# Optimization experiments

Hardware: AMD Instinct MI355X
Metric: run time of the kernel (lower is better)

Reference implementation:

```python
import jax, jax.numpy as jnp
import numpy as np

B, M, D, H = 2, 2048, 1024, 16


def _rope(x):
    # Equivalent to x.transpose(0,1) @ R[:m] with R the block-diagonal 2x2
    # rotation matrices from get_rotary_matrix (note the (i-1) in theta,
    # faithful to the source).
    b, m, d = x.shape
    i = jnp.arange(d // 2, dtype=jnp.float32)
    theta = 10000.0 ** (-2.0 * (i - 1.0) / d)           # [d/2]
    ang = jnp.arange(m, dtype=jnp.float32)[:, None] * theta[None, :]  # [m, d/2]
    c, s = jnp.cos(ang), jnp.sin(ang)
    xe, xo = x[..., 0::2], x[..., 1::2]                 # [b, m, d/2]
    ye = xe * c + xo * s                                # out[2i]   = q[2i]*cos + q[2i+1]*sin
    yo = -xe * s + xo * c                               # out[2i+1] = -q[2i]*sin + q[2i+1]*cos
    return jnp.stack([ye, yo], axis=-1).reshape(b, m, d)


def setup_inputs() -> dict:
    key = jax.random.key(0)
    ks = jax.random.split(key, 8)
    w = lambda k, shape: (jax.random.normal(k, shape, jnp.float32) * 0.02)
    return {
        "x": jax.random.normal(ks[0], (B, M, D), jnp.float32),
        "wq": w(ks[1], (D, D)),
        "wk": w(ks[2], (D, D)),
        "wv": w(ks[3], (D, D)),
        "in_proj_w": w(ks[4], (3 * D, D)),
        "in_proj_b": w(ks[5], (3 * D,)),
        "out_w": w(ks[6], (D, D)),
        "out_b": w(ks[7], (D,)),
    }


def reference(x, wq, wk, wv, in_proj_w, in_proj_b, out_w, out_b):
    b, m, d = x.shape
    h = H
    hd = d // h
    # bias-free QKV projections, each followed by the dense RoPE rotation
    q = _rope(x @ wq.T)
    k = _rope(x @ wk.T)
    v = _rope(x @ wv.T)
    # nn.MultiheadAttention: packed in_proj, scaled dot-product, causal mask, out_proj
    wqi, wki, wvi = jnp.split(in_proj_w, 3, axis=0)
    bqi, bki, bvi = jnp.split(in_proj_b, 3, axis=0)
    qh = (q @ wqi.T + bqi).reshape(b, m, h, hd)
    kh = (k @ wki.T + bki).reshape(b, m, h, hd)
    vh = (v @ wvi.T + bvi).reshape(b, m, h, hd)
    scores = jnp.einsum("bqhd,bkhd->bhqk", qh, kh) / jnp.sqrt(jnp.float32(hd))
    causal = jnp.tril(jnp.ones((m, m), dtype=bool))
    scores = jnp.where(causal, scores, jnp.float32(-jnp.inf))
    attn = jax.nn.softmax(scores, axis=-1)              # dropout p=0.0
    o = jnp.einsum("bhqk,bkhd->bqhd", attn, vh).reshape(b, m, d)
    return o @ out_w.T + out_b
```

## Files before the change

### kernel.cpp

```cpp
#include <hip/hip_runtime.h>
#include <hip/hip_bf16.h>
#include <math.h>

typedef __bf16 bf16;
typedef __bf16 bf16x4 __attribute__((ext_vector_type(4)));
typedef __bf16 bf16x8 __attribute__((ext_vector_type(8)));
typedef float  f32x4  __attribute__((ext_vector_type(4)));

#define MM 2048
#define DD 1024
#define HD 64

__device__ __forceinline__ void gload16(const void* g, void* l) {
  __builtin_amdgcn_global_load_lds((const __attribute__((address_space(1))) void*)g,
                                   (__attribute__((address_space(3))) void*)l, 16, 0, 0);
}

__global__ __launch_bounds__(256) void k_cvt_all(
    const float* __restrict__ x,   const float* __restrict__ wq,
    const float* __restrict__ wk,  const float* __restrict__ wv,
    const float* __restrict__ ipw, const float* __restrict__ ow,
    bf16* __restrict__ xb,  bf16* __restrict__ wqb, bf16* __restrict__ wkb,
    bf16* __restrict__ wvb, bf16* __restrict__ ipwb, bf16* __restrict__ owb)
{
  int bid = blockIdx.x;
  const float* s; bf16* d; int base;
  if (bid < 4096)       { s = x;   d = xb;   base = bid; }
  else if (bid < 5120)  { s = wq;  d = wqb;  base = bid - 4096; }
  else if (bid < 6144)  { s = wk;  d = wkb;  base = bid - 5120; }
  else if (bid < 7168)  { s = wv;  d = wvb;  base = bid - 6144; }
  else if (bid < 10240) { s = ipw; d = ipwb; base = bid - 7168; }
  else                  { s = ow;  d = owb;  base = bid - 10240; }
  int i = base*256 + threadIdx.x;
  float4 v = ((const float4*)s)[i];
  bf16x4 o;
  o[0]=(bf16)v.x; o[1]=(bf16)v.y; o[2]=(bf16)v.z; o[3]=(bf16)v.w;
  ((bf16x4*)d)[i] = o;
}

__device__ __forceinline__ void gemm_core(const bf16* __restrict__ A,
                                          const bf16* __restrict__ Bw,
                                          const int row0, const int col0,
                                          bf16* __restrict__ sA, bf16* __restrict__ sB,
                                          f32x4 (&acc)[4][4])
{
  const int t = threadIdx.x;
  #pragma unroll
  for (int m=0;m<4;m++)
    #pragma unroll
    for (int n=0;n<4;n++)
      acc[m][n] = (f32x4){0.f,0.f,0.f,0.f};

  const int srow = t >> 3;
  const int lch  = ((t & 7) - (srow & 7)) & 7;
  const bf16* gA = A  + (size_t)(row0 + srow)*DD + lch*8;
  const bf16* gB = Bw + (size_t)(col0 + srow)*DD + lch*8;
  char* lA = (char*)sA + t*16;
  char* lB = (char*)sB + t*16;

  const int lane = t & 63, wid = t >> 6;
  const int wr = wid >> 1, wc = wid & 1;
  const int fr = lane & 15, fg = lane >> 4;
  const int fr7 = fr & 7;

  #pragma unroll
  for (int jj=0;jj<4;jj++) gload16(gA + (size_t)jj*32*DD, lA + jj*4096);
  #pragma unroll
  for (int jj=0;jj<4;jj++) gload16(gB + (size_t)jj*32*DD, lB + jj*4096);

  for (int kt = 0; kt < 16; ++kt) {
    const int buf = kt & 1;
    __builtin_amdgcn_s_barrier();
    if (kt < 15) {
      const int nb = buf ^ 1;
      const int ko = (kt + 1) * 64;
      #pragma unroll
      for (int jj=0;jj<4;jj++) gload16(gA + (size_t)jj*32*DD + ko, lA + nb*16384 + jj*4096);
      #pragma unroll
      for (int jj=0;jj<4;jj++) gload16(gB + (size_t)jj*32*DD + ko, lB + nb*16384 + jj*4096);
      asm volatile("s_waitcnt vmcnt(8)" ::: "memory");
    } else {
      asm volatile("s_waitcnt vmcnt(0)" ::: "memory");
    }
    __builtin_amdgcn_s_barrier();
    const char* bA = (const char*)sA + buf*16384;
    const char* bB = (const char*)sB + buf*16384;
    bf16x8 aF[2][4], bF[2][4];
    #pragma unroll
    for (int kb=0;kb<2;kb++) {
      #pragma unroll
      for (int m=0;m<4;m++)
        aF[kb][m] = *(const bf16x8*)(bA + (wr*64 + m*16 + fr)*128 + ((kb*4 + fg + fr7)&7)*16);
      #pragma unroll
      for (int n=0;n<4;n++)
        bF[kb][n] = *(const bf16x8*)(bB + (wc*64 + n*16 + fr)*128 + ((kb*4 + fg + fr7)&7)*16);
    }
    __builtin_amdgcn_s_setprio(1);
    #pragma unroll
    for (int kb=0;kb<2;kb++)
      #pragma unroll
      for (int m=0;m<4;m++)
        #pragma unroll
        for (int n=0;n<4;n++)
          acc[m][n] = __builtin_amdgcn_mfma_f32_16x16x32_bf16(aF[kb][m], bF[kb][n], acc[m][n], 0, 0, 0);
    __builtin_amdgcn_s_setprio(0);
  }
}

__global__ __launch_bounds__(256, 2) void k_gemm_rope(
    const bf16* __restrict__ X, const bf16* __restrict__ Wq,
    const bf16* __restrict__ Wk, const bf16* __restrict__ Wv,
    bf16* __restrict__ QKV)
{
  __shared__ bf16 sA[2*128*64];
  __shared__ bf16 sB[2*128*64];
  const int row0 = blockIdx.x * 128;
  const int col0 = blockIdx.y * 128;
  const int z = blockIdx.z;
  const bf16* Bw = (z==0) ? Wq : ((z==1) ? Wk : Wv);
  f32x4 acc[4][4];
  gemm_core(X, Bw, row0, col0, sA, sB, acc);

  bf16* outp = QKV + (size_t)z * (4096u*1024u);
  const int lane = threadIdx.x & 63, wid = threadIdx.x >> 6;
  const int wr = wid >> 1, wc = wid & 1;
  const int fr = lane & 15, fg = lane >> 4;
  #pragma unroll
  for (int n=0;n<4;n++) {
    const int gc = col0 + wc*64 + n*16 + fr;
    const int i2 = gc >> 1;
    const float theta = __expf(((float)i2 - 1.0f) * (-2.0f * 9.210340371976184f / 1024.0f));
    #pragma unroll
    for (int m=0;m<4;m++) {
      #pragma unroll
      for (int r=0;r<4;r++) {
        const int gr = row0 + wr*64 + m*16 + fg*4 + r;
        const float v  = acc[m][n][r];
        const float pv = __shfl_xor(v, 1);
        const int pos = gr & (MM-1);
        float sv, cv;
        __sincosf((float)pos * theta, &sv, &cv);
        const float res = (gc & 1) ? (v*cv - pv*sv) : (v*cv + pv*sv);
        outp[(size_t)gr * DD + gc] = (bf16)res;
      }
    }
  }
}

__global__ __launch_bounds__(256, 2) void k_gemm_proj(
    const bf16* __restrict__ QKV, const bf16* __restrict__ IPW,
    const float* __restrict__ IPB,
    bf16* __restrict__ QH, bf16* __restrict__ KH, bf16* __restrict__ VT)
{
  __shared__ bf16 sA[2*128*64];
  __shared__ bf16 sB[2*128*64];
  const int row0 = blockIdx.x * 128;
  const int col0 = blockIdx.y * 128;
  const int z = blockIdx.z;
  const bf16* A  = QKV + (size_t)z * (4096u*1024u);
  const bf16* Bw = IPW + (size_t)z * (1024u*1024u);
  const float* bias = IPB + z * DD;
  f32x4 acc[4][4];
  gemm_core(A, Bw, row0, col0, sA, sB, acc);

  const int lane = threadIdx.x & 63, wid = threadIdx.x >> 6;
  const int wr = wid >> 1, wc = wid & 1;
  const int fr = lane & 15, fg = lane >> 4;
  if (z < 2) {
    bf16* outp = (z==0) ? QH : KH;
    const float vscale = (z==0) ? 0.18033688011112042f : 1.0f;
    #pragma unroll
    for (int n=0;n<4;n++) {
      const int gc = col0 + wc*64 + n*16 + fr;
      const float bs = bias[gc];
      #pragma unroll
      for (int m=0;m<4;m++) {
        #pragma unroll
        for (int r=0;r<4;r++) {
          const int gr = row0 + wr*64 + m*16 + fg*4 + r;
          outp[(size_t)gr * DD + gc] = (bf16)((acc[m][n][r] + bs) * vscale);
        }
      }
    }
  } else {
    #pragma unroll
    for (int n=0;n<4;n++) {
      const int gc = col0 + wc*64 + n*16 + fr;
      const float bs = bias[gc];
      #pragma unroll
      for (int m=0;m<4;m++) {
        const int gr0 = row0 + wr*64 + m*16 + fg*4;
        const int b  = gr0 >> 11;
        const int m0 = gr0 & (MM-1);
        bf16x4 pk;
        #pragma unroll
        for (int r=0;r<4;r++) pk[r] = (bf16)(acc[m][n][r] + bs);
        *(bf16x4*)(VT + ((size_t)b*DD + gc)*MM + m0) = pk;
      }
    }
  }
}

__global__ __launch_bounds__(256) void k_attn(
    const bf16* __restrict__ QH, const bf16* __restrict__ KH,
    const bf16* __restrict__ VT, bf16* __restrict__ O)
{
  __shared__ bf16 sK[2*64*64];
  __shared__ bf16 sV[2*64*64];
  __shared__ bf16 sP[4*16*64];
  const int idx = blockIdx.x;
  const int xcd = idx & 7;
  const int rr  = idx >> 3;
  const int combo = xcd*4 + (rr & 3);
  const int b = combo >> 4, h = combo & 15;
  const int pair = rr >> 2;
  const int t = threadIdx.x, lane = t & 63, wid = t >> 6;
  const int fr = lane & 15, fg = lane >> 4;
  const int swzP = (fr & 7) << 4;

  const int srow = t >> 3;
  const int cc   = (t & 7) ^ (srow & 7);
  const bf16* gK0 = KH + ((size_t)b*MM + srow)*DD + h*HD + cc*8;
  const bf16* gK1 = gK0 + (size_t)32*DD;
  const bf16* gV0 = VT + ((size_t)b*DD + h*HD + srow)*MM + cc*8;
  const bf16* gV1 = gV0 + (size_t)32*MM;
  char* lK = (char*)sK + t*16;
  char* lV = (char*)sV + t*16;
  char* sPw = (char*)(sP + wid*16*64);

  #pragma unroll 1
  for (int half = 0; half < 2; ++half) {
    const int qt = half ? pair : (31 - pair);
    const int q0 = qt * 64;
    const int qg = q0 + wid*16 + fr;

    const bf16* qp = QH + ((size_t)b*MM + qg)*DD + h*HD + fg*8;
    bf16x8 aQ0 = *(const bf16x8*)qp;
    bf16x8 aQ1 = *(const bf16x8*)(qp + 32);

    if (half) __builtin_amdgcn_s_barrier();

    gload16(gK0, lK);  gload16(gK1, lK + 4096);
    gload16(gV0, lV);  gload16(gV1, lV + 4096);

    f32x4 o_acc[4];
    #pragma unroll
    for (int n=0;n<4;n++) o_acc[n] = (f32x4){0.f,0.f,0.f,0.f};
    float mrow = -INFINITY, lrow = 0.f;

    for (int kt = 0; kt <= qt; ++kt) {
      const int buf = kt & 1;
      asm volatile("s_waitcnt vmcnt(0)" ::: "memory");
      __builtin_amdgcn_s_barrier();
      if (kt < qt) {
        const int nb = buf ^ 1;
        gload16(gK0 + (size_t)(kt+1)*64*DD, lK + nb*8192);
        gload16(gK1 + (size_t)(kt+1)*64*DD, lK + nb*8192 + 4096);
        gload16(gV0 + (kt+1)*64,            lV + nb*8192);
        gload16(gV1 + (kt+1)*64,            lV + nb*8192 + 4096);
      }
      const char* bKb = (const char*)sK + buf*8192;
      const char* bVb = (const char*)sV + buf*8192;

      f32x4 sacc[4];
      #pragma unroll
      for (int n=0;n<4;n++) sacc[n] = (f32x4){0.f,0.f,0.f,0.f};
      __builtin_amdgcn_s_setprio(1);
      #pragma unroll
      for (int kb=0;kb<2;kb++) {
        const bf16x8 q = kb ? aQ1 : aQ0;
        #pragma unroll
        for (int n=0;n<4;n++) {
          const int rowA = n*16 + fr;
          bf16x8 aK = *(const bf16x8*)(bKb + rowA*128 + ((kb*64 + fg*16) ^ ((rowA&7)<<4)));
          sacc[n] = __builtin_amdgcn_mfma_f32_16x16x32_bf16(aK, q, sacc[n], 0, 0, 0);
        }
      }
      __builtin_amdgcn_s_setprio(0);

      const bool diag = (kt == qt);
      float pv[16];
      #pragma unroll
      for (int n=0;n<4;n++)
        #pragma unroll
        for (int r=0;r<4;r++) {
          float xx = sacc[n][r];
          if (diag) {
            const int kvg = kt*64 + n*16 + fg*4 + r;
            if (kvg > qg) xx = -INFINITY;
          }
          pv[n*4+r] = xx;
        }
      float m8[8];
      #pragma unroll
      for (int i=0;i<8;i++) m8[i] = fmaxf(pv[i], pv[i+8]);
      #pragma unroll
      for (int i=0;i<4;i++) m8[i] = fmaxf(m8[i], m8[i+4]);
      float rmax = fmaxf(fmaxf(m8[0],m8[1]), fmaxf(m8[2],m8[3]));
      rmax = fmaxf(rmax, __shfl_xor(rmax, 16));
      rmax = fmaxf(rmax, __shfl_xor(rmax, 32));
      if (!__all(rmax - mrow <= 11.5f)) {
        const float mnew = fmaxf(mrow, rmax);
        const float scale = exp2f(mrow - mnew);
        mrow = mnew;
        lrow *= scale;
        float sc[4];
        #pragma unroll
        for (int r=0;r<4;r++) sc[r] = __shfl(scale, fg*4 + r);
        #pragma unroll
        for (int n=0;n<4;n++)
          #pragma unroll
          for (int r=0;r<4;r++) o_acc[n][r] *= sc[r];
      }
      float ps[16];
      #pragma unroll
      for (int i=0;i<16;i++) ps[i] = exp2f(pv[i] - mrow);
      #pragma unroll
      for (int n=0;n<4;n++) {
        bf16x4 pk;
        #pragma unroll
        for (int r=0;r<4;r++) pk[r] = (bf16)ps[n*4+r];
        *(bf16x4*)(sPw + fr*128 + ((n*32 + fg*8) ^ swzP)) = pk;
      }
      float s8[8];
      #pragma unroll
      for (int i=0;i<8;i++) s8[i] = ps[i] + ps[i+8];
      #pragma unroll
      for (int i=0;i<4;i++) s8[i] += s8[i+4];
      float rsum = (s8[0]+s8[1]) + (s8[2]+s8[3]);
      rsum += __shfl_xor(rsum, 16);
      rsum += __shfl_xor(rsum, 32);
      lrow += rsum;
      asm volatile("s_waitcnt lgkmcnt(0)" ::: "memory");

      bf16x8 aP0 = *(const bf16x8*)(sPw + fr*128 + ((fg*16) ^ swzP));
      bf16x8 aP1 = *(const bf16x8*)(sPw + fr*128 + ((64 + fg*16) ^ swzP));
      __builtin_amdgcn_s_setprio(1);
      #pragma unroll
      for (int n=0;n<4;n++) {
        const int rowV = n*16 + fr;
        bf16x8 bV0 = *(const bf16x8*)(bVb + rowV*128 + ((fg*16) ^ ((rowV&7)<<4)));
        bf16x8 bV1 = *(const bf16x8*)(bVb + rowV*128 + ((64 + fg*16) ^ ((rowV&7)<<4)));
        o_acc[n] = __builtin_amdgcn_mfma_f32_16x16x32_bf16(aP0, bV0, o_acc[n], 0, 0, 0);
        o_acc[n] = __builtin_amdgcn_mfma_f32_16x16x32_bf16(aP1, bV1, o_acc[n], 0, 0, 0);
      }
      __builtin_amdgcn_s_setprio(0);
    }

    const float linv = 1.0f / lrow;
    float inv4[4];
    #pragma unroll
    for (int r=0;r<4;r++) inv4[r] = __shfl(linv, fg*4 + r);
    #pragma unroll
    for (int r=0;r<4;r++) {
      const int qq = q0 + wid*16 + fg*4 + r;
      #pragma unroll
      for (int n=0;n<4;n++) {
        O[((size_t)b*MM + qq)*DD + h*HD + n*16 + fr] = (bf16)(o_acc[n][r] * inv4[r]);
      }
    }
  }
}

__global__ __launch_bounds__(256, 2) void k_gemm_out(
    const bf16* __restrict__ A, const bf16* __restrict__ OW,
    const float* __restrict__ OBIAS, float* __restrict__ outp)
{
  __shared__ bf16 sA[2*128*64];
  __shared__ bf16 sB[2*128*64];
  const int row0 = blockIdx.x * 128;
  const int col0 = blockIdx.y * 128;
  f32x4 acc[4][4];
  gemm_core(A, OW, row0, col0, sA, sB, acc);
  const int lane = threadIdx.x & 63, wid = threadIdx.x >> 6;
  const int wr = wid >> 1, wc = wid & 1;
  const int fr = lane & 15, fg = lane >> 4;
  #pragma unroll
  for (int n=0;n<4;n++) {
    const int gc = col0 + wc*64 + n*16 + fr;
    const float bs = OBIAS[gc];
    #pragma unroll
    for (int m=0;m<4;m++) {
      #pragma unroll
      for (int r=0;r<4;r++) {
        const int gr = row0 + wr*64 + m*16 + fg*4 + r;
        outp[(size_t)gr * DD + gc] = acc[m][n][r] + bs;
      }
    }
  }
}

extern "C" void kernel_launch(void* const* d_in, const int* in_sizes, int n_in,
                              void* d_out, int out_size, void* d_ws, size_t ws_size,
                              hipStream_t stream)
{
  (void)in_sizes; (void)n_in; (void)out_size; (void)ws_size;
  const float* x   = (const float*)d_in[0];
  const float* wq  = (const float*)d_in[1];
  const float* wk  = (const float*)d_in[2];
  const float* wv  = (const float*)d_in[3];
  const float* ipw = (const float*)d_in[4];
  const float* ipb = (const float*)d_in[5];
  const float* ow  = (const float*)d_in[6];
  const float* ob  = (const float*)d_in[7];
  float* outp = (float*)d_out;

  char* ws = (char*)d_ws;
  const size_t MB = 1u << 20;
  bf16* xb   = (bf16*)(ws + 0*MB);
  bf16* wqb  = (bf16*)(ws + 8*MB);
  bf16* wkb  = (bf16*)(ws + 10*MB);
  bf16* wvb  = (bf16*)(ws + 12*MB);
  bf16* ipwb = (bf16*)(ws + 14*MB);
  bf16* owb  = (bf16*)(ws + 20*MB);
  bf16* QKV  = (bf16*)(ws + 22*MB);
  bf16* QH   = (bf16*)(ws + 46*MB);
  bf16* KH   = (bf16*)(ws + 54*MB);
  bf16* VT   = (bf16*)(ws + 62*MB);
  bf16* Ob   = (bf16*)(ws + 70*MB);

  k_cvt_all<<<11264, 256, 0, stream>>>(x, wq, wk, wv, ipw, ow,
                                       xb, wqb, wkb, wvb, ipwb, owb);
  k_gemm_rope<<<dim3(32,8,3), 256, 0, stream>>>(xb, wqb, wkb, wvb, QKV);
  k_gemm_proj<<<dim3(32,8,3), 256, 0, stream>>>(QKV, ipwb, ipb, QH, KH, VT);
  k_attn<<<512, 256, 0, stream>>>(QH, KH, VT, Ob);
  k_gemm_out<<<dim3(32,8,1), 256, 0, stream>>>(Ob, owb, ob, outp);
}
```

Baseline: 157.8 us.

## Use 8-wave GEMM blocks and one query tile per attention block

The shared GEMM core now runs with 512 threads (8 waves) per 128x128 tile. Each wave computes a 32x64 sub-tile instead of 64x64, and each thread issues half as many global-to-LDS loads per stage. The attention kernel no longer pairs a long and a short causal query tile in one block; it launches 1024 blocks, each handling a single query tile in descending tile order. The aim is more waves in flight and finer-grained scheduling, at the cost of less register-level reuse per wave in the GEMMs and the loss of the explicit causal load balancing from pairing.

```diff
diff --git a/kernel.cpp b/kernel.cpp
--- a/kernel.cpp
+++ b/kernel.cpp
@@ -38,15 +38,15 @@
   ((bf16x4*)d)[i] = o;
 }
 
-__device__ __forceinline__ void gemm_core(const bf16* __restrict__ A,
-                                          const bf16* __restrict__ Bw,
-                                          const int row0, const int col0,
-                                          bf16* __restrict__ sA, bf16* __restrict__ sB,
-                                          f32x4 (&acc)[4][4])
+__device__ __forceinline__ void gemm_core8(const bf16* __restrict__ A,
+                                           const bf16* __restrict__ Bw,
+                                           const int row0, const int col0,
+                                           bf16* __restrict__ sA, bf16* __restrict__ sB,
+                                           f32x4 (&acc)[2][4])
 {
   const int t = threadIdx.x;
   #pragma unroll
-  for (int m=0;m<4;m++)
+  for (int m=0;m<2;m++)
     #pragma unroll
     for (int n=0;n<4;n++)
       acc[m][n] = (f32x4){0.f,0.f,0.f,0.f};
@@ -63,10 +63,10 @@
   const int fr = lane & 15, fg = lane >> 4;
   const int fr7 = fr & 7;
 
-  #pragma unroll
-  for (int jj=0;jj<4;jj++) gload16(gA + (size_t)jj*32*DD, lA + jj*4096);
-  #pragma unroll
-  for (int jj=0;jj<4;jj++) gload16(gB + (size_t)jj*32*DD, lB + jj*4096);
+  gload16(gA,                 lA);
+  gload16(gA + (size_t)64*DD, lA + 8192);
+  gload16(gB,                 lB);
+  gload16(gB + (size_t)64*DD, lB + 8192);
 
   for (int kt = 0; kt < 16; ++kt) {
     const int buf = kt & 1;
@@ -74,23 +74,23 @@
     if (kt < 15) {
       const int nb = buf ^ 1;
       const int ko = (kt + 1) * 64;
-      #pragma unroll
-      for (int jj=0;jj<4;jj++) gload16(gA + (size_t)jj*32*DD + ko, lA + nb*16384 + jj*4096);
-      #pragma unroll
-      for (int jj=0;jj<4;jj++) gload16(gB + (size_t)jj*32*DD + ko, lB + nb*16384 + jj*4096);
-      asm volatile("s_waitcnt vmcnt(8)" ::: "memory");
+      gload16(gA + ko,                 lA + nb*16384);
+      gload16(gA + (size_t)64*DD + ko, lA + nb*16384 + 8192);
+      gload16(gB + ko,                 lB + nb*16384);
+      gload16(gB + (size_t)64*DD + ko, lB + nb*16384 + 8192);
+      asm volatile("s_waitcnt vmcnt(4)" ::: "memory");
     } else {
       asm volatile("s_waitcnt vmcnt(0)" ::: "memory");
     }
     __builtin_amdgcn_s_barrier();
     const char* bA = (const char*)sA + buf*16384;
     const char* bB = (const char*)sB + buf*16384;
-    bf16x8 aF[2][4], bF[2][4];
+    bf16x8 aF[2][2], bF[2][4];
     #pragma unroll
     for (int kb=0;kb<2;kb++) {
       #pragma unroll
-      for (int m=0;m<4;m++)
-        aF[kb][m] = *(const bf16x8*)(bA + (wr*64 + m*16 + fr)*128 + ((kb*4 + fg + fr7)&7)*16);
+      for (int m=0;m<2;m++)
+        aF[kb][m] = *(const bf16x8*)(bA + (wr*32 + m*16 + fr)*128 + ((kb*4 + fg + fr7)&7)*16);
       #pragma unroll
       for (int n=0;n<4;n++)
         bF[kb][n] = *(const bf16x8*)(bB + (wc*64 + n*16 + fr)*128 + ((kb*4 + fg + fr7)&7)*16);
@@ -99,7 +99,7 @@
     #pragma unroll
     for (int kb=0;kb<2;kb++)
       #pragma unroll
-      for (int m=0;m<4;m++)
+      for (int m=0;m<2;m++)
         #pragma unroll
         for (int n=0;n<4;n++)
           acc[m][n] = __builtin_amdgcn_mfma_f32_16x16x32_bf16(aF[kb][m], bF[kb][n], acc[m][n], 0, 0, 0);
@@ -107,7 +107,7 @@
   }
 }
 
-__global__ __launch_bounds__(256, 2) void k_gemm_rope(
+__global__ __launch_bounds__(512, 2) void k_gemm_rope(
     const bf16* __restrict__ X, const bf16* __restrict__ Wq,
     const bf16* __restrict__ Wk, const bf16* __restrict__ Wv,
     bf16* __restrict__ QKV)
@@ -118,8 +118,8 @@
   const int col0 = blockIdx.y * 128;
   const int z = blockIdx.z;
   const bf16* Bw = (z==0) ? Wq : ((z==1) ? Wk : Wv);
-  f32x4 acc[4][4];
-  gemm_core(X, Bw, row0, col0, sA, sB, acc);
+  f32x4 acc[2][4];
+  gemm_core8(X, Bw, row0, col0, sA, sB, acc);
 
   bf16* outp = QKV + (size_t)z * (4096u*1024u);
   const int lane = threadIdx.x & 63, wid = threadIdx.x >> 6;
@@ -131,10 +131,10 @@
     const int i2 = gc >> 1;
     const float theta = __expf(((float)i2 - 1.0f) * (-2.0f * 9.210340371976184f / 1024.0f));
     #pragma unroll
-    for (int m=0;m<4;m++) {
+    for (int m=0;m<2;m++) {
       #pragma unroll
       for (int r=0;r<4;r++) {
-        const int gr = row0 + wr*64 + m*16 + fg*4 + r;
+        const int gr = row0 + wr*32 + m*16 + fg*4 + r;
         const float v  = acc[m][n][r];
         const float pv = __shfl_xor(v, 1);
         const int pos = gr & (MM-1);
@@ -147,7 +147,7 @@
   }
 }
 
-__global__ __launch_bounds__(256, 2) void k_gemm_proj(
+__global__ __launch_bounds__(512, 2) void k_gemm_proj(
     const bf16* __restrict__ QKV, const bf16* __restrict__ IPW,
     const float* __restrict__ IPB,
     bf16* __restrict__ QH, bf16* __restrict__ KH, bf16* __restrict__ VT)
@@ -160,8 +160,8 @@
   const bf16* A  = QKV + (size_t)z * (4096u*1024u);
   const bf16* Bw = IPW + (size_t)z * (1024u*1024u);
   const float* bias = IPB + z * DD;
-  f32x4 acc[4][4];
-  gemm_core(A, Bw, row0, col0, sA, sB, acc);
+  f32x4 acc[2][4];
+  gemm_core8(A, Bw, row0, col0, sA, sB, acc);
 
   const int lane = threadIdx.x & 63, wid = threadIdx.x >> 6;
   const int wr = wid >> 1, wc = wid & 1;
@@ -174,10 +174,10 @@
       const int gc = col0 + wc*64 + n*16 + fr;
       const float bs = bias[gc];
       #pragma unroll
-      for (int m=0;m<4;m++) {
+      for (int m=0;m<2;m++) {
         #pragma unroll
         for (int r=0;r<4;r++) {
-          const int gr = row0 + wr*64 + m*16 + fg*4 + r;
+          const int gr = row0 + wr*32 + m*16 + fg*4 + r;
           outp[(size_t)gr * DD + gc] = (bf16)((acc[m][n][r] + bs) * vscale);
         }
       }
@@ -188,8 +188,8 @@
       const int gc = col0 + wc*64 + n*16 + fr;
       const float bs = bias[gc];
       #pragma unroll
-      for (int m=0;m<4;m++) {
-        const int gr0 = row0 + wr*64 + m*16 + fg*4;
+      for (int m=0;m<2;m++) {
+        const int gr0 = row0 + wr*32 + m*16 + fg*4;
         const int b  = gr0 >> 11;
         const int m0 = gr0 & (MM-1);
         bf16x4 pk;
@@ -213,10 +213,12 @@
   const int rr  = idx >> 3;
   const int combo = xcd*4 + (rr & 3);
   const int b = combo >> 4, h = combo & 15;
-  const int pair = rr >> 2;
+  const int qt = 31 - (rr >> 2);
   const int t = threadIdx.x, lane = t & 63, wid = t >> 6;
   const int fr = lane & 15, fg = lane >> 4;
   const int swzP = (fr & 7) << 4;
+  const int q0 = qt * 64;
+  const int qg = q0 + wid*16 + fr;
 
   const int srow = t >> 3;
   const int cc   = (t & 7) ^ (srow & 7);
@@ -228,141 +230,132 @@
   char* lV = (char*)sV + t*16;
   char* sPw = (char*)(sP + wid*16*64);
 
-  #pragma unroll 1
-  for (int half = 0; half < 2; ++half) {
-    const int qt = half ? pair : (31 - pair);
-    const int q0 = qt * 64;
-    const int qg = q0 + wid*16 + fr;
-
-    const bf16* qp = QH + ((size_t)b*MM + qg)*DD + h*HD + fg*8;
-    bf16x8 aQ0 = *(const bf16x8*)qp;
-    bf16x8 aQ1 = *(const bf16x8*)(qp + 32);
-
-    if (half) __builtin_amdgcn_s_barrier();
-
-    gload16(gK0, lK);  gload16(gK1, lK + 4096);
-    gload16(gV0, lV);  gload16(gV1, lV + 4096);
-
-    f32x4 o_acc[4];
-    #pragma unroll
-    for (int n=0;n<4;n++) o_acc[n] = (f32x4){0.f,0.f,0.f,0.f};
-    float mrow = -INFINITY, lrow = 0.f;
-
-    for (int kt = 0; kt <= qt; ++kt) {
-      const int buf = kt & 1;
-      asm volatile("s_waitcnt vmcnt(0)" ::: "memory");
-      __builtin_amdgcn_s_barrier();
-      if (kt < qt) {
-        const int nb = buf ^ 1;
-        gload16(gK0 + (size_t)(kt+1)*64*DD, lK + nb*8192);
-        gload16(gK1 + (size_t)(kt+1)*64*DD, lK + nb*8192 + 4096);
-        gload16(gV0 + (kt+1)*64,            lV + nb*8192);
-        gload16(gV1 + (kt+1)*64,            lV + nb*8192 + 4096);
-      }
-      const char* bKb = (const char*)sK + buf*8192;
-      const char* bVb = (const char*)sV + buf*8192;
-
-      f32x4 sacc[4];
-      #pragma unroll
-      for (int n=0;n<4;n++) sacc[n] = (f32x4){0.f,0.f,0.f,0.f};
-      __builtin_amdgcn_s_setprio(1);
-      #pragma unroll
-      for (int kb=0;kb<2;kb++) {
-        const bf16x8 q = kb ? aQ1 : aQ0;
-        #pragma unroll
-        for (int n=0;n<4;n++) {
-          const int rowA = n*16 + fr;
-          bf16x8 aK = *(const bf16x8*)(bKb + rowA*128 + ((kb*64 + fg*16) ^ ((rowA&7)<<4)));
-          sacc[n] = __builtin_amdgcn_mfma_f32_16x16x32_bf16(aK, q, sacc[n], 0, 0, 0);
+  const bf16* qp = QH + ((size_t)b*MM + qg)*DD + h*HD + fg*8;
+  bf16x8 aQ0 = *(const bf16x8*)qp;
+  bf16x8 aQ1 = *(const bf16x8*)(qp + 32);
+
+  gload16(gK0, lK);  gload16(gK1, lK + 4096);
+  gload16(gV0, lV);  gload16(gV1, lV + 4096);
+
+  f32x4 o_acc[4];
+  #pragma unroll
+  for (int n=0;n<4;n++) o_acc[n] = (f32x4){0.f,0.f,0.f,0.f};
+  float mrow = -INFINITY, lrow = 0.f;
+
+  for (int kt = 0; kt <= qt; ++kt) {
+    const int buf = kt & 1;
+    asm volatile("s_waitcnt vmcnt(0)" ::: "memory");
+    __builtin_amdgcn_s_barrier();
+    if (kt < qt) {
+      const int nb = buf ^ 1;
+      gload16(gK0 + (size_t)(kt+1)*64*DD, lK + nb*8192);
+      gload16(gK1 + (size_t)(kt+1)*64*DD, lK + nb*8192 + 4096);
+      gload16(gV0 + (kt+1)*64,            lV + nb*8192);
+      gload16(gV1 + (kt+1)*64,            lV + nb*8192 + 4096);
+    }
+    const char* bKb = (const char*)sK + buf*8192;
+    const char* bVb = (const char*)sV + buf*8192;
+
+    f32x4 sacc[4];
+    #pragma unroll
+    for (int n=0;n<4;n++) sacc[n] = (f32x4){0.f,0.f,0.f,0.f};
+    __builtin_amdgcn_s_setprio(1);
+    #pragma unroll
+    for (int kb=0;kb<2;kb++) {
+      const bf16x8 q = kb ? aQ1 : aQ0;
+      #pragma unroll
+      for (int n=0;n<4;n++) {
+        const int rowA = n*16 + fr;
+        bf16x8 aK = *(const bf16x8*)(bKb + rowA*128 + ((kb*64 + fg*16) ^ ((rowA&7)<<4)));
+        sacc[n] = __builtin_amdgcn_mfma_f32_16x16x32_bf16(aK, q, sacc[n], 0, 0, 0);
+      }
+    }
+    __builtin_amdgcn_s_setprio(0);
+
+    const bool diag = (kt == qt);
+    float pv[16];
+    #pragma unroll
+    for (int n=0;n<4;n++)
+      #pragma unroll
+      for (int r=0;r<4;r++) {
+        float xx = sacc[n][r];
+        if (diag) {
+          const int kvg = kt*64 + n*16 + fg*4 + r;
+          if (kvg > qg) xx = -INFINITY;
         }
-      }
-      __builtin_amdgcn_s_setprio(0);
-
-      const bool diag = (kt == qt);
-      float pv[16];
+        pv[n*4+r] = xx;
+      }
+    float m8[8];
+    #pragma unroll
+    for (int i=0;i<8;i++) m8[i] = fmaxf(pv[i], pv[i+8]);
+    #pragma unroll
+    for (int i=0;i<4;i++) m8[i] = fmaxf(m8[i], m8[i+4]);
+    float rmax = fmaxf(fmaxf(m8[0],m8[1]), fmaxf(m8[2],m8[3]));
+    rmax = fmaxf(rmax, __shfl_xor(rmax, 16));
+    rmax = fmaxf(rmax, __shfl_xor(rmax, 32));
+    if (!__all(rmax - mrow <= 11.5f)) {
+      const float mnew = fmaxf(mrow, rmax);
+      const float scale = exp2f(mrow - mnew);
+      mrow = mnew;
+      lrow *= scale;
+      float sc[4];
+      #pragma unroll
+      for (int r=0;r<4;r++) sc[r] = __shfl(scale, fg*4 + r);
       #pragma unroll
       for (int n=0;n<4;n++)
         #pragma unroll
-        for (int r=0;r<4;r++) {
-          float xx = sacc[n][r];
-          if (diag) {
-            const int kvg = kt*64 + n*16 + fg*4 + r;
-            if (kvg > qg) xx = -INFINITY;
-          }
-          pv[n*4+r] = xx;
-        }
-      float m8[8];
-      #pragma unroll
-      for (int i=0;i<8;i++) m8[i] = fmaxf(pv[i], pv[i+8]);
-      #pragma unroll
-      for (int i=0;i<4;i++) m8[i] = fmaxf(m8[i], m8[i+4]);
-      float rmax = fmaxf(fmaxf(m8[0],m8[1]), fmaxf(m8[2],m8[3]));
-      rmax = fmaxf(rmax, __shfl_xor(rmax, 16));
-      rmax = fmaxf(rmax, __shfl_xor(rmax, 32));
-      if (!__all(rmax - mrow <= 11.5f)) {
-        const float mnew = fmaxf(mrow, rmax);
-        const float scale = exp2f(mrow - mnew);
-        mrow = mnew;
-        lrow *= scale;
-        float sc[4];
-        #pragma unroll
-        for (int r=0;r<4;r++) sc[r] = __shfl(scale, fg*4 + r);
-        #pragma unroll
-        for (int n=0;n<4;n++)
-          #pragma unroll
-          for (int r=0;r<4;r++) o_acc[n][r] *= sc[r];
-      }
-      float ps[16];
-      #pragma unroll
-      for (int i=0;i<16;i++) ps[i] = exp2f(pv[i] - mrow);
-      #pragma unroll
-      for (int n=0;n<4;n++) {
-        bf16x4 pk;
-        #pragma unroll
-        for (int r=0;r<4;r++) pk[r] = (bf16)ps[n*4+r];
-        *(bf16x4*)(sPw + fr*128 + ((n*32 + fg*8) ^ swzP)) = pk;
-      }
-      float s8[8];
-      #pragma unroll
-      for (int i=0;i<8;i++) s8[i] = ps[i] + ps[i+8];
-      #pragma unroll
-      for (int i=0;i<4;i++) s8[i] += s8[i+4];
-      float rsum = (s8[0]+s8[1]) + (s8[2]+s8[3]);
-      rsum += __shfl_xor(rsum, 16);
-      rsum += __shfl_xor(rsum, 32);
-      lrow += rsum;
-      asm volatile("s_waitcnt lgkmcnt(0)" ::: "memory");
-
-      bf16x8 aP0 = *(const bf16x8*)(sPw + fr*128 + ((fg*16) ^ swzP));
-      bf16x8 aP1 = *(const bf16x8*)(sPw + fr*128 + ((64 + fg*16) ^ swzP));
-      __builtin_amdgcn_s_setprio(1);
-      #pragma unroll
-      for (int n=0;n<4;n++) {
-        const int rowV = n*16 + fr;
-        bf16x8 bV0 = *(const bf16x8*)(bVb + rowV*128 + ((fg*16) ^ ((rowV&7)<<4)));
-        bf16x8 bV1 = *(const bf16x8*)(bVb + rowV*128 + ((64 + fg*16) ^ ((rowV&7)<<4)));
-        o_acc[n] = __builtin_amdgcn_mfma_f32_16x16x32_bf16(aP0, bV0, o_acc[n], 0, 0, 0);
-        o_acc[n] = __builtin_amdgcn_mfma_f32_16x16x32_bf16(aP1, bV1, o_acc[n], 0, 0, 0);
-      }
-      __builtin_amdgcn_s_setprio(0);
-    }
-
-    const float linv = 1.0f / lrow;
-    float inv4[4];
-    #pragma unroll
-    for (int r=0;r<4;r++) inv4[r] = __shfl(linv, fg*4 + r);
-    #pragma unroll
-    for (int r=0;r<4;r++) {
-      const int qq = q0 + wid*16 + fg*4 + r;
-      #pragma unroll
-      for (int n=0;n<4;n++) {
-        O[((size_t)b*MM + qq)*DD + h*HD + n*16 + fr] = (bf16)(o_acc[n][r] * inv4[r]);
-      }
-    }
-  }
-}
-
-__global__ __launch_bounds__(256, 2) void k_gemm_out(
+        for (int r=0;r<4;r++) o_acc[n][r] *= sc[r];
+    }
+    float ps[16];
+    #pragma unroll
+    for (int i=0;i<16;i++) ps[i] = exp2f(pv[i] - mrow);
+    #pragma unroll
+    for (int n=0;n<4;n++) {
+      bf16x4 pk;
+      #pragma unroll
+      for (int r=0;r<4;r++) pk[r] = (bf16)ps[n*4+r];
+      *(bf16x4*)(sPw + fr*128 + ((n*32 + fg*8) ^ swzP)) = pk;
+    }
+    float s8[8];
+    #pragma unroll
+    for (int i=0;i<8;i++) s8[i] = ps[i] + ps[i+8];
+    #pragma unroll
+    for (int i=0;i<4;i++) s8[i] += s8[i+4];
+    float rsum = (s8[0]+s8[1]) + (s8[2]+s8[3]);
+    rsum += __shfl_xor(rsum, 16);
+    rsum += __shfl_xor(rsum, 32);
+    lrow += rsum;
+    asm volatile("s_waitcnt lgkmcnt(0)" ::: "memory");
+
+    bf16x8 aP0 = *(const bf16x8*)(sPw + fr*128 + ((fg*16) ^ swzP));
+    bf16x8 aP1 = *(const bf16x8*)(sPw + fr*128 + ((64 + fg*16) ^ swzP));
+    __builtin_amdgcn_s_setprio(1);
+    #pragma unroll
+    for (int n=0;n<4;n++) {
+      const int rowV = n*16 + fr;
+      bf16x8 bV0 = *(const bf16x8*)(bVb + rowV*128 + ((fg*16) ^ ((rowV&7)<<4)));
+      bf16x8 bV1 = *(const bf16x8*)(bVb + rowV*128 + ((64 + fg*16) ^ ((rowV&7)<<4)));
+      o_acc[n] = __builtin_amdgcn_mfma_f32_16x16x32_bf16(aP0, bV0, o_acc[n], 0, 0, 0);
+      o_acc[n] = __builtin_amdgcn_mfma_f32_16x16x32_bf16(aP1, bV1, o_acc[n], 0, 0, 0);
+    }
+    __builtin_amdgcn_s_setprio(0);
+  }
+
+  const float linv = 1.0f / lrow;
+  float inv4[4];
+  #pragma unroll
+  for (int r=0;r<4;r++) inv4[r] = __shfl(linv, fg*4 + r);
+  #pragma unroll
+  for (int r=0;r<4;r++) {
+    const int qq = q0 + wid*16 + fg*4 + r;
+    #pragma unroll
+    for (int n=0;n<4;n++) {
+      O[((size_t)b*MM + qq)*DD + h*HD + n*16 + fr] = (bf16)(o_acc[n][r] * inv4[r]);
+    }
+  }
+}
+
+__global__ __launch_bounds__(512, 2) void k_gemm_out(
     const bf16* __restrict__ A, const bf16* __restrict__ OW,
     const float* __restrict__ OBIAS, float* __restrict__ outp)
 {
@@ -370,8 +363,8 @@
   __shared__ bf16 sB[2*128*64];
   const int row0 = blockIdx.x * 128;
   const int col0 = blockIdx.y * 128;
-  f32x4 acc[4][4];
-  gemm_core(A, OW, row0, col0, sA, sB, acc);
+  f32x4 acc[2][4];
+  gemm_core8(A, OW, row0, col0, sA, sB, acc);
   const int lane = threadIdx.x & 63, wid = threadIdx.x >> 6;
   const int wr = wid >> 1, wc = wid & 1;
   const int fr = lane & 15, fg = lane >> 4;
@@ -380,10 +373,10 @@
     const int gc = col0 + wc*64 + n*16 + fr;
     const float bs = OBIAS[gc];
     #pragma unroll
-    for (int m=0;m<4;m++) {
+    for (int m=0;m<2;m++) {
       #pragma unroll
       for (int r=0;r<4;r++) {
-        const int gr = row0 + wr*64 + m*16 + fg*4 + r;
+        const int gr = row0 + wr*32 + m*16 + fg*4 + r;
         outp[(size_t)gr * DD + gc] = acc[m][n][r] + bs;
       }
     }
@@ -421,8 +414,8 @@
 
   k_cvt_all<<<11264, 256, 0, stream>>>(x, wq, wk, wv, ipw, ow,
                                        xb, wqb, wkb, wvb, ipwb, owb);
-  k_gemm_rope<<<dim3(32,8,3), 256, 0, stream>>>(xb, wqb, wkb, wvb, QKV);
-  k_gemm_proj<<<dim3(32,8,3), 256, 0, stream>>>(QKV, ipwb, ipb, QH, KH, VT);
-  k_attn<<<512, 256, 0, stream>>>(QH, KH, VT, Ob);
-  k_gemm_out<<<dim3(32,8,1), 256, 0, stream>>>(Ob, owb, ob, outp);
-}
+  k_gemm_rope<<<dim3(32,8,3), 512, 0, stream>>>(xb, wqb, wkb, wvb, QKV);
+  k_gemm_proj<<<dim3(32,8,3), 512, 0, stream>>>(QKV, ipwb, ipb, QH, KH, VT);
+  k_attn<<<1024, 256, 0, stream>>>(QH, KH, VT, Ob);
+  k_gemm_out<<<dim3(32,8,1), 512, 0, stream>>>(Ob, owb, ob, outp);
+}
```

New measurement: 138.1 us. 1.14x faster.
